# Performance work log

Hardware: AMD Instinct MI355X
Metric: run time of the kernel (lower is better)

## Reference

```python
import jax, jax.numpy as jnp
import numpy as np

K = 128          # num_clusters (init kwarg k)
N_ITERS = 100    # torch loop runs up to 100 iters; converged centroids are a
                 # fixed point, so running all 100 matches the early-exit result


def _sq_dists(x, c):
    # squared Euclidean distances [N, K]; argmin identical to torch.cdist argmin
    return (jnp.sum(x * x, axis=1, keepdims=True)
            - 2.0 * (x @ c.T)
            + jnp.sum(c * c, axis=1)[None, :])


def _assign_and_update(x, c):
    ids = jnp.argmin(_sq_dists(x, c), axis=1)                     # [N]
    sums = jax.ops.segment_sum(x, ids, num_segments=K)            # [K, D]
    counts = jax.ops.segment_sum(jnp.ones((x.shape[0],), x.dtype), ids,
                                 num_segments=K)                  # [K]
    return ids, sums / counts[:, None]   # mean per cluster (NaN if empty, as in torch)


def setup_inputs() -> dict:
    key = jax.random.key(0)
    kx, kp = jax.random.split(key)
    N, D = 32768, 256
    x = jax.random.normal(kx, (N, D), dtype=jnp.float32)
    # torch.randperm(N)[:K] -> distinct initial centroid indices
    init_idx = jax.random.permutation(kp, N)[:K].astype(jnp.int32)
    return {"x": x, "init_idx": init_idx}


def reference(x, init_idx):
    c0 = x[init_idx]  # [K, D]

    def body(c, _):
        _, newc = _assign_and_update(x, c)
        return newc, None

    # 99 updates, then final assignment + update: returned ids correspond to the
    # centroids BEFORE the last update, exactly like the torch loop's last iter.
    c, _ = jax.lax.scan(body, c0, None, length=N_ITERS - 1)
    ids, c = _assign_and_update(x, c)

    logits = x @ c.T  # temperature = 1.0
    logp = jax.nn.log_softmax(logits, axis=-1)
    # CrossEntropyLoss(mean) with pseudo labels = cluster ids
    loss = -jnp.mean(jnp.take_along_axis(logp, ids[:, None], axis=1))
    return loss
```

## Files before the change

### kernel.cpp

```cpp
#include <hip/hip_runtime.h>
#include <cstdint>

#define NPTS 32768
#define DIM  256
#define NK   128
#define NITER 100
#define NBLK 256
#define NTHR 1024
#define PAD  33

typedef unsigned short ushort_t;
typedef unsigned long long ull_t;
typedef __attribute__((ext_vector_type(8))) short s8v;
typedef __attribute__((ext_vector_type(4))) float f4v;

__device__ __forceinline__ unsigned short f2bf(float f) {
  unsigned u = __float_as_uint(f);
  u += 0x7fffu + ((u >> 16) & 1u);
  return (unsigned short)(u >> 16);
}
__device__ __forceinline__ float bf2f(unsigned short b) {
  return __uint_as_float(((unsigned)b) << 16);
}

__device__ __forceinline__ void cstore(float* p, float v) {
  __hip_atomic_store(p, v, __ATOMIC_RELAXED, __HIP_MEMORY_SCOPE_AGENT);
}
__device__ __forceinline__ float cload(const float* p) {
  return __hip_atomic_load(p, __ATOMIC_RELAXED, __HIP_MEMORY_SCOPE_AGENT);
}
__device__ __forceinline__ void cstorei(int* p, int v) {
  __hip_atomic_store(p, v, __ATOMIC_RELAXED, __HIP_MEMORY_SCOPE_AGENT);
}
__device__ __forceinline__ int cloadi(const int* p) {
  return __hip_atomic_load(p, __ATOMIC_RELAXED, __HIP_MEMORY_SCOPE_AGENT);
}
__device__ __forceinline__ void cstore64(ull_t* p, ull_t v) {
  __hip_atomic_store(p, v, __ATOMIC_RELAXED, __HIP_MEMORY_SCOPE_AGENT);
}
__device__ __forceinline__ ull_t cload64(const ull_t* p) {
  return __hip_atomic_load(p, __ATOMIC_RELAXED, __HIP_MEMORY_SCOPE_AGENT);
}

__device__ __forceinline__ void stage4(const ushort_t* __restrict__ src, s8v* buf, int h, int t) {
  const int lane = t & 63;
  const int wb = (t >> 6) << 6;
#pragma unroll
  for (int i = 0; i < 2; ++i) {
    const int Gb = i * 1024 + wb;
    const int G  = Gb + lane;
    const int Gs = G ^ ((G >> 4) & 7);
    const char* ga = (const char*)src + (G >> 4) * 512 + h * 256 + (Gs & 15) * 16;
    __builtin_amdgcn_global_load_lds(
        (const __attribute__((address_space(1))) void*)ga,
        (__attribute__((address_space(3))) void*)((char*)buf + Gb * 16),
        16, 0, 0);
  }
}

__device__ __forceinline__ void stage_c(const ull_t* __restrict__ cpk,
                                        s8v* bh, s8v* bl, int h, int t) {
#pragma unroll
  for (int i = 0; i < 2; ++i) {
    const int G = i * NTHR + t;
    const int k = G >> 4, gcol = G & 15;
    const int sc2 = gcol ^ (k & 7);
    const ull_t* src = cpk + (size_t)k * 128 + h * 64 + sc2 * 4;
    ull_t w0 = cload64(src + 0), w1 = cload64(src + 1);
    ull_t w2 = cload64(src + 2), w3 = cload64(src + 3);
    s8v vh, vl;
    vh[0] = (short)w0; vl[0] = (short)(w0 >> 16); vh[1] = (short)(w0 >> 32); vl[1] = (short)(w0 >> 48);
    vh[2] = (short)w1; vl[2] = (short)(w1 >> 16); vh[3] = (short)(w1 >> 32); vl[3] = (short)(w1 >> 48);
    vh[4] = (short)w2; vl[4] = (short)(w2 >> 16); vh[5] = (short)(w2 >> 32); vl[5] = (short)(w2 >> 48);
    vh[6] = (short)w3; vl[6] = (short)(w3 >> 16); vh[7] = (short)(w3 >> 32); vl[7] = (short)(w3 >> 48);
    *(s8v*)((char*)bh + G * 16) = vh;
    *(s8v*)((char*)bl + G * 16) = vl;
  }
}

__device__ __forceinline__ void gbar(unsigned* flags, unsigned gen) {
  __syncthreads();
  if (threadIdx.x == 0)
    __hip_atomic_store(&flags[blockIdx.x * 16], gen, __ATOMIC_RELAXED, __HIP_MEMORY_SCOPE_AGENT);
  if (threadIdx.x < NBLK) {
    while (__hip_atomic_load(&flags[threadIdx.x * 16], __ATOMIC_RELAXED, __HIP_MEMORY_SCOPE_AGENT) < gen)
      __builtin_amdgcn_s_sleep(1);
  }
  asm volatile("" ::: "memory");
  __syncthreads();
}
__device__ __forceinline__ void gbar_pf(unsigned* flags, unsigned gen,
    const ushort_t* xhb, const ushort_t* xlb, s8v (*bufs)[2048], int t) {
  __syncthreads();
  stage4(xhb, bufs[0], 0, t);
  stage4(xlb, bufs[1], 0, t);
  if (t == 0)
    __hip_atomic_store(&flags[blockIdx.x * 16], gen, __ATOMIC_RELAXED, __HIP_MEMORY_SCOPE_AGENT);
  if (t < NBLK) {
    while (__hip_atomic_load(&flags[t * 16], __ATOMIC_RELAXED, __HIP_MEMORY_SCOPE_AGENT) < gen)
      __builtin_amdgcn_s_sleep(1);
  }
  asm volatile("" ::: "memory");
  __syncthreads();
}

struct SMa {
  s8v bufs[4][2048];
  float cns[NK];
  float redd[NK * 4];
  int   redk[NK * 4];
  float gmaxs[NK];
  float labvs[NK];
  int   labis[NK];
};
union ScU {
  float accB[NK * PAD];
  float red4[1024];
  float redcn[1024];
};

__device__ __forceinline__ void gemm_core(
    SMa& sm, int t,
    const ushort_t* __restrict__ xhb, const ushort_t* __restrict__ xlb,
    const ull_t* __restrict__ cpk, const float* __restrict__ cn, f4v (&acc)[2][2]) {
  const int lane = t & 63;
  const int w    = t >> 6;
  const int wr   = w >> 2, wc = w & 3;
  const int g    = lane >> 4, lr = lane & 15;

  if (t < NK) sm.cns[t] = cload(&cn[t]);

  const f4v zero = {0.f, 0.f, 0.f, 0.f};
#pragma unroll
  for (int i = 0; i < 2; ++i)
#pragma unroll
    for (int j = 0; j < 2; ++j) acc[i][j] = zero;

  const int swz = (lr & 7) << 4;
  int a_off[2], b_off[2];
#pragma unroll
  for (int i = 0; i < 2; ++i) a_off[i] = (wr * 32 + i * 16 + lr) * 256 + g * 16;
#pragma unroll
  for (int j = 0; j < 2; ++j) b_off[j] = (wc * 32 + j * 16 + lr) * 256 + g * 16;

  for (int h = 0; h < 2; ++h) {
    if (h == 1) {
      stage4(xhb, sm.bufs[0], 1, t);
      stage4(xlb, sm.bufs[1], 1, t);
    }
    stage_c(cpk, sm.bufs[2], sm.bufs[3], h, t);
    __syncthreads();
#pragma unroll
    for (int kk = 0; kk < 4; ++kk) {
      s8v ah[2], al[2], bh[2], bl[2];
#pragma unroll
      for (int i = 0; i < 2; ++i) {
        int o = (a_off[i] + kk * 64) ^ swz;
        ah[i] = *(const s8v*)((const char*)sm.bufs[0] + o);
        al[i] = *(const s8v*)((const char*)sm.bufs[1] + o);
      }
#pragma unroll
      for (int j = 0; j < 2; ++j) {
        int o = (b_off[j] + kk * 64) ^ swz;
        bh[j] = *(const s8v*)((const char*)sm.bufs[2] + o);
        bl[j] = *(const s8v*)((const char*)sm.bufs[3] + o);
      }
#pragma unroll
      for (int i = 0; i < 2; ++i)
#pragma unroll
        for (int j = 0; j < 2; ++j) {
          acc[i][j] = __builtin_amdgcn_mfma_f32_16x16x32_bf16(ah[i], bh[j], acc[i][j], 0, 0, 0);
          acc[i][j] = __builtin_amdgcn_mfma_f32_16x16x32_bf16(ah[i], bl[j], acc[i][j], 0, 0, 0);
          acc[i][j] = __builtin_amdgcn_mfma_f32_16x16x32_bf16(al[i], bh[j], acc[i][j], 0, 0, 0);
        }
    }
    if (h == 0) __syncthreads();
  }
}

__global__ __launch_bounds__(NTHR, 1) void kmeans_fused(
    const float* __restrict__ x, const int* __restrict__ init_idx,
    ushort_t* __restrict__ xh, ushort_t* __restrict__ xl,
    ull_t* __restrict__ cpk, float* __restrict__ cn, int* __restrict__ ids,
    float* __restrict__ psum, float* __restrict__ pcnt,
    float* __restrict__ outp, unsigned* __restrict__ flags,
    float* __restrict__ out) {
  __shared__ SMa sm;
  __shared__ ScU sc;
  __shared__ int idslB[1024];
  __shared__ int cntB[NK];
  __shared__ ushort_t hsm[DIM], lsm[DIM];
  __shared__ float cntsh;

  const int b = blockIdx.x;
  const int t = threadIdx.x;
  const int lane = t & 63;
  const int w  = t >> 6;
  const int wr = w >> 2, wc = w & 3;
  const int g  = lane >> 4, lr = lane & 15;
  const int pbase = b * 128;
  const ushort_t* xhb = xh + (size_t)pbase * DIM;
  const ushort_t* xlb = xl + (size_t)pbase * DIM;
  unsigned gen = 1;

  for (int i = 0; i < 4; ++i) {
    int gg = b * 4096 + i * NTHR + t;
    const float4* src = (const float4*)x + gg * 2;
    float4 fa = src[0], fb = src[1];
    float vv[8] = {fa.x, fa.y, fa.z, fa.w, fb.x, fb.y, fb.z, fb.w};
    s8v vh, vl;
#pragma unroll
    for (int j = 0; j < 8; ++j) {
      unsigned short hh = f2bf(vv[j]);
      vh[j] = (short)hh;
      vl[j] = (short)f2bf(vv[j] - bf2f(hh));
    }
    ((s8v*)xh)[gg] = vh;
    ((s8v*)xl)[gg] = vl;
  }

  if (b < NK) {
    float eff = 0.f;
    if (t < DIM) {
      float v = x[init_idx[b] * DIM + t];
      unsigned short hh = f2bf(v);
      unsigned short ll = f2bf(v - bf2f(hh));
      hsm[t] = hh; lsm[t] = ll;
      eff = bf2f(hh) + bf2f(ll);
    }
    __syncthreads();
    sc.redcn[t] = (t < DIM) ? eff * eff : 0.f;
    if (t < NK) {
      ull_t wv = (ull_t)hsm[2 * t] | ((ull_t)lsm[2 * t] << 16)
               | ((ull_t)hsm[2 * t + 1] << 32) | ((ull_t)lsm[2 * t + 1] << 48);
      cstore64(&cpk[(size_t)b * 128 + t], wv);
    }
    __syncthreads();
    for (int s = 512; s > 0; s >>= 1) { if (t < s) sc.redcn[t] += sc.redcn[t + s]; __syncthreads(); }
    if (t == 0) cstore(&cn[b], sc.redcn[0]);
  }
  gbar_pf(flags, gen, xhb, xlb, sm.bufs, t); ++gen;

  for (int it = 0; it < NITER; ++it) {
    {
      f4v acc[2][2];
      gemm_core(sm, t, xhb, xlb, cpk, cn, acc);
#pragma unroll
      for (int i = 0; i < 2; ++i) {
#pragma unroll
        for (int r = 0; r < 4; ++r) {
          int prow = wr * 32 + i * 16 + g * 4 + r;
          float bd = 1e30f; int bk = 0;
#pragma unroll
          for (int j = 0; j < 2; ++j) {
            int col = wc * 32 + j * 16 + lr;
            float s = sm.cns[col] - 2.f * acc[i][j][r];
            if (s < bd || (s == bd && col < bk)) { bd = s; bk = col; }
          }
#pragma unroll
          for (int msk = 1; msk < 16; msk <<= 1) {
            float od = __shfl_xor(bd, msk, 64);
            int   ok = __shfl_xor(bk, msk, 64);
            if (od < bd || (od == bd && ok < bk)) { bd = od; bk = ok; }
          }
          if (lr == 0) { sm.redd[prow * 4 + wc] = bd; sm.redk[prow * 4 + wc] = bk; }
        }
      }
      __syncthreads();
      if (t < NK) {
        float bd = sm.redd[t * 4]; int bk = sm.redk[t * 4];
#pragma unroll
        for (int q = 1; q < 4; ++q) {
          float dq = sm.redd[t * 4 + q]; int kq = sm.redk[t * 4 + q];
          if (dq < bd || (dq == bd && kq < bk)) { bd = dq; bk = kq; }
        }
        cstorei(&ids[pbase + t], bk);
      }
    }
    gbar(flags, gen); ++gen;

    {
      const int pg = b & 31, dg = b >> 5;
      for (int i = t; i < NK * PAD; i += NTHR) sc.accB[i] = 0.f;
      if (t < NK) cntB[t] = 0;
      idslB[t] = cloadi(&ids[pg * 1024 + t]);
      __syncthreads();
      const int id = idslB[t];
      if (dg == 0) atomicAdd(&cntB[id], 1);
      const float* xr = x + ((size_t)pg * 1024 + t) * DIM + dg * 32;
      f4v v0 = __builtin_nontemporal_load((const f4v*)xr + 0);
      f4v v1 = __builtin_nontemporal_load((const f4v*)xr + 1);
      f4v v2 = __builtin_nontemporal_load((const f4v*)xr + 2);
      f4v v3 = __builtin_nontemporal_load((const f4v*)xr + 3);
      f4v v4 = __builtin_nontemporal_load((const f4v*)xr + 4);
      f4v v5 = __builtin_nontemporal_load((const f4v*)xr + 5);
      f4v v6 = __builtin_nontemporal_load((const f4v*)xr + 6);
      f4v v7 = __builtin_nontemporal_load((const f4v*)xr + 7);
      float* ab = &sc.accB[id * PAD];
      atomicAdd(ab + 0,  v0[0]); atomicAdd(ab + 1,  v0[1]); atomicAdd(ab + 2,  v0[2]); atomicAdd(ab + 3,  v0[3]);
      atomicAdd(ab + 4,  v1[0]); atomicAdd(ab + 5,  v1[1]); atomicAdd(ab + 6,  v1[2]); atomicAdd(ab + 7,  v1[3]);
      atomicAdd(ab + 8,  v2[0]); atomicAdd(ab + 9,  v2[1]); atomicAdd(ab + 10, v2[2]); atomicAdd(ab + 11, v2[3]);
      atomicAdd(ab + 12, v3[0]); atomicAdd(ab + 13, v3[1]); atomicAdd(ab + 14, v3[2]); atomicAdd(ab + 15, v3[3]);
      atomicAdd(ab + 16, v4[0]); atomicAdd(ab + 17, v4[1]); atomicAdd(ab + 18, v4[2]); atomicAdd(ab + 19, v4[3]);
      atomicAdd(ab + 20, v5[0]); atomicAdd(ab + 21, v5[1]); atomicAdd(ab + 22, v5[2]); atomicAdd(ab + 23, v5[3]);
      atomicAdd(ab + 24, v6[0]); atomicAdd(ab + 25, v6[1]); atomicAdd(ab + 26, v6[2]); atomicAdd(ab + 27, v6[3]);
      atomicAdd(ab + 28, v7[0]); atomicAdd(ab + 29, v7[1]); atomicAdd(ab + 30, v7[2]); atomicAdd(ab + 31, v7[3]);
      __syncthreads();
#pragma unroll
      for (int s2 = 0; s2 < 4; ++s2) {
        int idx = s2 * NTHR + t;
        int k2 = idx >> 5, dl = idx & 31;
        cstore(&psum[(((size_t)dg * NK + k2) * 32 + pg) * 32 + dl], sc.accB[k2 * PAD + dl]);
      }
      if (dg == 0 && t < NK)
        cstore(&pcnt[(size_t)pg * NK + t], (float)cntB[t]);
    }
    gbar(flags, gen); ++gen;

    if (b < NK) {
      const int k = b;
      const int hf = t >> 8, tt = t & 255;
      const int dgc = tt >> 5, dlc = tt & 31;
      float s = 0.f;
#pragma unroll
      for (int p2 = hf * 8; p2 < hf * 8 + 8; ++p2)
        s += cload(&psum[(((size_t)dgc * NK + k) * 32 + p2) * 32 + dlc]);
      sc.red4[hf * 256 + tt] = s;
      float cv = (t < 32) ? cload(&pcnt[(size_t)t * NK + k]) : 0.f;
      if (t < 64) {
#pragma unroll
        for (int m = 1; m < 32; m <<= 1) cv += __shfl_xor(cv, m, 64);
      }
      if (t == 0) cntsh = cv;
      __syncthreads();
      float eff = 0.f;
      if (t < DIM) {
        float mean = (sc.red4[t] + sc.red4[256 + t] + sc.red4[512 + t] + sc.red4[768 + t]) / cntsh;
        unsigned short hh = f2bf(mean);
        unsigned short ll = f2bf(mean - bf2f(hh));
        hsm[t] = hh; lsm[t] = ll;
        eff = bf2f(hh) + bf2f(ll);
      }
      __syncthreads();
      sc.redcn[t] = (t < DIM) ? eff * eff : 0.f;
      if (t < NK) {
        ull_t wv = (ull_t)hsm[2 * t] | ((ull_t)lsm[2 * t] << 16)
                 | ((ull_t)hsm[2 * t + 1] << 32) | ((ull_t)lsm[2 * t + 1] << 48);
        cstore64(&cpk[(size_t)k * 128 + t], wv);
      }
      __syncthreads();
      for (int st = 512; st > 0; st >>= 1) { if (t < st) sc.redcn[t] += sc.redcn[t + st]; __syncthreads(); }
      if (t == 0) cstore(&cn[k], sc.redcn[0]);
    }
    gbar_pf(flags, gen, xhb, xlb, sm.bufs, t); ++gen;
  }

  {
    f4v acc[2][2];
    gemm_core(sm, t, xhb, xlb, cpk, cn, acc);
#pragma unroll
    for (int i = 0; i < 2; ++i) {
#pragma unroll
      for (int r = 0; r < 4; ++r) {
        int prow = wr * 32 + i * 16 + g * 4 + r;
        float m = -1e30f;
#pragma unroll
        for (int j = 0; j < 2; ++j) m = fmaxf(m, acc[i][j][r]);
#pragma unroll
        for (int msk = 1; msk < 16; msk <<= 1) m = fmaxf(m, __shfl_xor(m, msk, 64));
        if (lr == 0) sm.redd[prow * 4 + wc] = m;
      }
    }
    __syncthreads();
    if (t < NK) {
      float m = sm.redd[t * 4];
#pragma unroll
      for (int q = 1; q < 4; ++q) m = fmaxf(m, sm.redd[t * 4 + q]);
      sm.gmaxs[t] = m;
      sm.labis[t] = cloadi(&ids[pbase + t]);
    }
    __syncthreads();
#pragma unroll
    for (int i = 0; i < 2; ++i) {
#pragma unroll
      for (int r = 0; r < 4; ++r) {
        int prow = wr * 32 + i * 16 + g * 4 + r;
        float m = sm.gmaxs[prow];
        int lab = sm.labis[prow];
        float s = 0.f;
#pragma unroll
        for (int j = 0; j < 2; ++j) {
          int col = wc * 32 + j * 16 + lr;
          float v = acc[i][j][r];
          s += expf(v - m);
          if (col == lab) sm.labvs[prow] = v;
        }
#pragma unroll
        for (int msk = 1; msk < 16; msk <<= 1) s += __shfl_xor(s, msk, 64);
        if (lr == 0) sm.redd[prow * 4 + wc] = s;
      }
    }
    __syncthreads();
    if (t < NK) {
      float se = sm.redd[t * 4] + sm.redd[t * 4 + 1] + sm.redd[t * 4 + 2] + sm.redd[t * 4 + 3];
      float lse = sm.gmaxs[t] + logf(se);
      sm.gmaxs[t] = lse - sm.labvs[t];
    }
    __syncthreads();
    if (t == 0) {
      float tot = 0.f;
      for (int q = 0; q < NK; ++q) tot += sm.gmaxs[q];
      cstore(&outp[b], tot);
    }
  }
  gbar(flags, gen); ++gen;
  if (b == 0) {
    sc.redcn[t] = (t < NBLK) ? cload(&outp[t]) : 0.f;
    __syncthreads();
    for (int s = 512; s > 0; s >>= 1) { if (t < s) sc.redcn[t] += sc.redcn[t + s]; __syncthreads(); }
    if (t == 0) out[0] = sc.redcn[0] * (1.0f / (float)NPTS);
  }
}

extern "C" void kernel_launch(void* const* d_in, const int* in_sizes, int n_in,
                              void* d_out, int out_size, void* d_ws, size_t ws_size,
                              hipStream_t stream) {
  const float* x        = (const float*)d_in[0];
  const int*   init_idx = (const int*)d_in[1];
  float* out = (float*)d_out;
  char* ws = (char*)d_ws;

  ushort_t* xh  = (ushort_t*)(ws);
  ushort_t* xl  = (ushort_t*)(ws + 16777216);
  ull_t* cpk  = (ull_t*)(ws + 33554432);
  float* cn   = (float*)(ws + 33685504);
  int*   ids  = (int*)(ws + 33686016);
  float* psum = (float*)(ws + 33817088);
  float* pcnt = (float*)(ws + 38011392);
  float* outp = (float*)(ws + 38027776);
  unsigned* flags = (unsigned*)(ws + 38028800);

  hipMemsetAsync(flags, 0, 16384, stream);
  kmeans_fused<<<dim3(NBLK), dim3(NTHR), 0, stream>>>(
      x, init_idx, xh, xl, cpk, cn, ids, psum, pcnt, outp, flags, out);
}
```

Measured before the change: 7.250 ms.

## Split centroid update across all blocks with per-half norms and move prefetch barrier

```diff
diff --git a/kernel.cpp b/kernel.cpp
--- a/kernel.cpp
+++ b/kernel.cpp
@@ -40,6 +40,13 @@
 }
 __device__ __forceinline__ ull_t cload64(const ull_t* p) {
   return __hip_atomic_load(p, __ATOMIC_RELAXED, __HIP_MEMORY_SCOPE_AGENT);
+}
+__device__ __forceinline__ f4v cload128f(const ull_t* p) {
+  ull_t a = cload64(p), b = cload64(p + 1);
+  f4v r;
+  r[0] = __uint_as_float((unsigned)a); r[1] = __uint_as_float((unsigned)(a >> 32));
+  r[2] = __uint_as_float((unsigned)b); r[3] = __uint_as_float((unsigned)(b >> 32));
+  return r;
 }
 
 __device__ __forceinline__ void stage4(const ushort_t* __restrict__ src, s8v* buf, int h, int t) {
@@ -84,7 +91,7 @@
     __hip_atomic_store(&flags[blockIdx.x * 16], gen, __ATOMIC_RELAXED, __HIP_MEMORY_SCOPE_AGENT);
   if (threadIdx.x < NBLK) {
     while (__hip_atomic_load(&flags[threadIdx.x * 16], __ATOMIC_RELAXED, __HIP_MEMORY_SCOPE_AGENT) < gen)
-      __builtin_amdgcn_s_sleep(1);
+      __builtin_amdgcn_s_sleep(2);
   }
   asm volatile("" ::: "memory");
   __syncthreads();
@@ -98,7 +105,7 @@
     __hip_atomic_store(&flags[blockIdx.x * 16], gen, __ATOMIC_RELAXED, __HIP_MEMORY_SCOPE_AGENT);
   if (t < NBLK) {
     while (__hip_atomic_load(&flags[t * 16], __ATOMIC_RELAXED, __HIP_MEMORY_SCOPE_AGENT) < gen)
-      __builtin_amdgcn_s_sleep(1);
+      __builtin_amdgcn_s_sleep(2);
   }
   asm volatile("" ::: "memory");
   __syncthreads();
@@ -122,13 +129,13 @@
 __device__ __forceinline__ void gemm_core(
     SMa& sm, int t,
     const ushort_t* __restrict__ xhb, const ushort_t* __restrict__ xlb,
-    const ull_t* __restrict__ cpk, const float* __restrict__ cn, f4v (&acc)[2][2]) {
+    const ull_t* __restrict__ cpk, const float* __restrict__ cn2, f4v (&acc)[2][2]) {
   const int lane = t & 63;
   const int w    = t >> 6;
   const int wr   = w >> 2, wc = w & 3;
   const int g    = lane >> 4, lr = lane & 15;
 
-  if (t < NK) sm.cns[t] = cload(&cn[t]);
+  if (t < NK) sm.cns[t] = cload(&cn2[2 * t]) + cload(&cn2[2 * t + 1]);
 
   const f4v zero = {0.f, 0.f, 0.f, 0.f};
 #pragma unroll
@@ -181,7 +188,7 @@
 __global__ __launch_bounds__(NTHR, 1) void kmeans_fused(
     const float* __restrict__ x, const int* __restrict__ init_idx,
     ushort_t* __restrict__ xh, ushort_t* __restrict__ xl,
-    ull_t* __restrict__ cpk, float* __restrict__ cn, int* __restrict__ ids,
+    ull_t* __restrict__ cpk, float* __restrict__ cn2, int* __restrict__ ids,
     float* __restrict__ psum, float* __restrict__ pcnt,
     float* __restrict__ outp, unsigned* __restrict__ flags,
     float* __restrict__ out) {
@@ -237,14 +244,14 @@
     }
     __syncthreads();
     for (int s = 512; s > 0; s >>= 1) { if (t < s) sc.redcn[t] += sc.redcn[t + s]; __syncthreads(); }
-    if (t == 0) cstore(&cn[b], sc.redcn[0]);
+    if (t == 0) { cstore(&cn2[b * 2], sc.redcn[0]); cstore(&cn2[b * 2 + 1], 0.f); }
   }
   gbar_pf(flags, gen, xhb, xlb, sm.bufs, t); ++gen;
 
   for (int it = 0; it < NITER; ++it) {
     {
       f4v acc[2][2];
-      gemm_core(sm, t, xhb, xlb, cpk, cn, acc);
+      gemm_core(sm, t, xhb, xlb, cpk, cn2, acc);
 #pragma unroll
       for (int i = 0; i < 2; ++i) {
 #pragma unroll
@@ -287,15 +294,15 @@
       __syncthreads();
       const int id = idslB[t];
       if (dg == 0) atomicAdd(&cntB[id], 1);
-      const float* xr = x + ((size_t)pg * 1024 + t) * DIM + dg * 32;
-      f4v v0 = __builtin_nontemporal_load((const f4v*)xr + 0);
-      f4v v1 = __builtin_nontemporal_load((const f4v*)xr + 1);
-      f4v v2 = __builtin_nontemporal_load((const f4v*)xr + 2);
-      f4v v3 = __builtin_nontemporal_load((const f4v*)xr + 3);
-      f4v v4 = __builtin_nontemporal_load((const f4v*)xr + 4);
-      f4v v5 = __builtin_nontemporal_load((const f4v*)xr + 5);
-      f4v v6 = __builtin_nontemporal_load((const f4v*)xr + 6);
-      f4v v7 = __builtin_nontemporal_load((const f4v*)xr + 7);
+      const ull_t* xr = (const ull_t*)(x + ((size_t)pg * 1024 + t) * DIM + dg * 32);
+      f4v v0 = cload128f(xr + 0);
+      f4v v1 = cload128f(xr + 2);
+      f4v v2 = cload128f(xr + 4);
+      f4v v3 = cload128f(xr + 6);
+      f4v v4 = cload128f(xr + 8);
+      f4v v5 = cload128f(xr + 10);
+      f4v v6 = cload128f(xr + 12);
+      f4v v7 = cload128f(xr + 14);
       float* ab = &sc.accB[id * PAD];
       atomicAdd(ab + 0,  v0[0]); atomicAdd(ab + 1,  v0[1]); atomicAdd(ab + 2,  v0[2]); atomicAdd(ab + 3,  v0[3]);
       atomicAdd(ab + 4,  v1[0]); atomicAdd(ab + 5,  v1[1]); atomicAdd(ab + 6,  v1[2]); atomicAdd(ab + 7,  v1[3]);
@@ -315,17 +322,17 @@
       if (dg == 0 && t < NK)
         cstore(&pcnt[(size_t)pg * NK + t], (float)cntB[t]);
     }
-    gbar(flags, gen); ++gen;
-
-    if (b < NK) {
-      const int k = b;
-      const int hf = t >> 8, tt = t & 255;
-      const int dgc = tt >> 5, dlc = tt & 31;
+    gbar_pf(flags, gen, xhb, xlb, sm.bufs, t); ++gen;
+
+    {
+      const int k = b >> 1, hh2 = b & 1;
+      const int dwh = t & 127, pch = t >> 7;
+      const int dgc = hh2 * 4 + (dwh >> 5), dlc = dwh & 31;
       float s = 0.f;
 #pragma unroll
-      for (int p2 = hf * 8; p2 < hf * 8 + 8; ++p2)
+      for (int p2 = pch * 4; p2 < pch * 4 + 4; ++p2)
         s += cload(&psum[(((size_t)dgc * NK + k) * 32 + p2) * 32 + dlc]);
-      sc.red4[hf * 256 + tt] = s;
+      sc.red4[pch * 128 + dwh] = s;
       float cv = (t < 32) ? cload(&pcnt[(size_t)t * NK + k]) : 0.f;
       if (t < 64) {
 #pragma unroll
@@ -334,30 +341,33 @@
       if (t == 0) cntsh = cv;
       __syncthreads();
       float eff = 0.f;
-      if (t < DIM) {
-        float mean = (sc.red4[t] + sc.red4[256 + t] + sc.red4[512 + t] + sc.red4[768 + t]) / cntsh;
+      if (t < 128) {
+        float ssum = 0.f;
+#pragma unroll
+        for (int ww = 0; ww < 8; ++ww) ssum += sc.red4[ww * 128 + t];
+        float mean = ssum / cntsh;
         unsigned short hh = f2bf(mean);
         unsigned short ll = f2bf(mean - bf2f(hh));
         hsm[t] = hh; lsm[t] = ll;
         eff = bf2f(hh) + bf2f(ll);
       }
       __syncthreads();
-      sc.redcn[t] = (t < DIM) ? eff * eff : 0.f;
-      if (t < NK) {
+      sc.redcn[t] = (t < 128) ? eff * eff : 0.f;
+      if (t < 64) {
         ull_t wv = (ull_t)hsm[2 * t] | ((ull_t)lsm[2 * t] << 16)
                  | ((ull_t)hsm[2 * t + 1] << 32) | ((ull_t)lsm[2 * t + 1] << 48);
-        cstore64(&cpk[(size_t)k * 128 + t], wv);
+        cstore64(&cpk[(size_t)k * 128 + hh2 * 64 + t], wv);
       }
       __syncthreads();
       for (int st = 512; st > 0; st >>= 1) { if (t < st) sc.redcn[t] += sc.redcn[t + st]; __syncthreads(); }
-      if (t == 0) cstore(&cn[k], sc.redcn[0]);
-    }
-    gbar_pf(flags, gen, xhb, xlb, sm.bufs, t); ++gen;
+      if (t == 0) cstore(&cn2[k * 2 + hh2], sc.redcn[0]);
+    }
+    gbar(flags, gen); ++gen;
   }
 
   {
     f4v acc[2][2];
-    gemm_core(sm, t, xhb, xlb, cpk, cn, acc);
+    gemm_core(sm, t, xhb, xlb, cpk, cn2, acc);
 #pragma unroll
     for (int i = 0; i < 2; ++i) {
 #pragma unroll
@@ -433,14 +443,14 @@
   ushort_t* xh  = (ushort_t*)(ws);
   ushort_t* xl  = (ushort_t*)(ws + 16777216);
   ull_t* cpk  = (ull_t*)(ws + 33554432);
-  float* cn   = (float*)(ws + 33685504);
-  int*   ids  = (int*)(ws + 33686016);
-  float* psum = (float*)(ws + 33817088);
-  float* pcnt = (float*)(ws + 38011392);
-  float* outp = (float*)(ws + 38027776);
-  unsigned* flags = (unsigned*)(ws + 38028800);
+  float* cn2  = (float*)(ws + 33685504);
+  int*   ids  = (int*)(ws + 33686528);
+  float* psum = (float*)(ws + 33817600);
+  float* pcnt = (float*)(ws + 38011904);
+  float* outp = (float*)(ws + 38028288);
+  unsigned* flags = (unsigned*)(ws + 38029312);
 
   hipMemsetAsync(flags, 0, 16384, stream);
   kmeans_fused<<<dim3(NBLK), dim3(NTHR), 0, stream>>>(
-      x, init_idx, xh, xl, cpk, cn, ids, psum, pcnt, outp, flags, out);
-}
+      x, init_idx, xh, xl, cpk, cn2, ids, psum, pcnt, outp, flags, out);
+}
```

Measured after the change: 7.153 ms. Within noise of the previous version (-1.3%).
